# Performance work log

Measured on AMD Instinct MI355X. Metric: run time of the kernel, lower is better.

Reference implementation:

```python
import jax, jax.numpy as jnp
import numpy as np

N_NODES = 50000
N_EDGES = 800000
HIDDEN = 128
N_REL = 64
NUM_HEADS = 8
HEAD_DIM = HIDDEN // NUM_HEADS


def setup_inputs() -> dict:
    key = jax.random.key(0)
    ks = jax.random.split(key, 20)
    s = 0.05
    inp = {
        "x": jax.random.normal(ks[0], (N_NODES, HIDDEN), dtype=jnp.float32),
        "timestamps": jax.random.uniform(ks[1], (N_NODES,), dtype=jnp.float32),
        "src": jax.random.randint(ks[2], (N_EDGES,), 0, N_NODES),
        "dst": jax.random.randint(ks[3], (N_EDGES,), 0, N_NODES),
        "edge_type": jax.random.randint(ks[4], (N_EDGES,), 0, N_REL),
        "edge_time": jax.random.uniform(ks[5], (N_EDGES,), dtype=jnp.float32),
        # parameters (torch Linear stored as [in, out] so we use x @ W + b)
        "rel_table": jax.random.normal(ks[6], (N_REL, HIDDEN), dtype=jnp.float32) * s,
        "Wq": jax.random.normal(ks[7], (HIDDEN, HIDDEN), dtype=jnp.float32) * s,
        "bq": jnp.zeros((HIDDEN,), dtype=jnp.float32),
        "Wk": jax.random.normal(ks[8], (HIDDEN, HIDDEN), dtype=jnp.float32) * s,
        "bk": jnp.zeros((HIDDEN,), dtype=jnp.float32),
        "Wv": jax.random.normal(ks[9], (HIDDEN, HIDDEN), dtype=jnp.float32) * s,
        "bv": jnp.zeros((HIDDEN,), dtype=jnp.float32),
        "W1": jax.random.normal(ks[10], (2 * HIDDEN + 1, HIDDEN), dtype=jnp.float32) * s,
        "b1": jnp.zeros((HIDDEN,), dtype=jnp.float32),
        "W2": jax.random.normal(ks[11], (HIDDEN, 1), dtype=jnp.float32) * s,
        "b2": jnp.zeros((1,), dtype=jnp.float32),
        "time_coeff": jnp.array(1.0, dtype=jnp.float32),
    }
    return inp


def reference(x, timestamps, src, dst, edge_type, edge_time, rel_table,
              Wq, bq, Wk, bk, Wv, bv, W1, b1, W2, b2, time_coeff):
    N = x.shape[0]
    # temporal gating
    delta_t = (timestamps[dst] - edge_time) / (jnp.abs(time_coeff) + 1e-9)  # [E]
    time_mask = jax.nn.sigmoid(delta_t)[:, None]                            # [E,1]
    rel_emb = rel_table[edge_type] * time_mask                              # [E,H]
    src_emb = x[src]                                                        # [E,H]
    # dynamic edge weights: MLP([src_emb, rel_emb, time_mask]) -> sigmoid
    weight_input = jnp.concatenate([src_emb, rel_emb, time_mask], axis=-1)  # [E,2H+1]
    h = jax.nn.relu(weight_input @ W1 + b1)
    dynamic_weights = jax.nn.sigmoid(h @ W2 + b2)                           # [E,1]
    message = src_emb * rel_emb * dynamic_weights                           # [E,H]
    # multi-head edge attention keyed by dst
    q = (x[dst] @ Wq + bq).reshape(-1, NUM_HEADS, HEAD_DIM)
    k = (message @ Wk + bk).reshape(-1, NUM_HEADS, HEAD_DIM)
    v = (message @ Wv + bv).reshape(-1, NUM_HEADS, HEAD_DIM)
    scores = (q * k).sum(-1) / (HEAD_DIM ** 0.5)                            # [E,heads]
    # scatter softmax over edges grouped by dst
    seg_max = jax.ops.segment_max(scores, dst, num_segments=N)              # [N,heads]
    e = jnp.exp(scores - seg_max[dst])
    denom = jax.ops.segment_sum(e, dst, num_segments=N)
    attn = e / denom[dst]                                                   # [E,heads]
    out = jax.ops.segment_sum(v * attn[..., None], dst, num_segments=N)     # [N,heads,hd]
    return out.reshape(N, NUM_HEADS * HEAD_DIM)
```

## Files before the change

kernel.cpp:

```cpp
#include <hip/hip_runtime.h>

typedef __bf16 v8bf __attribute__((ext_vector_type(8)));
typedef __bf16 v4bf __attribute__((ext_vector_type(4)));
typedef float  v4f  __attribute__((ext_vector_type(4)));

#define MFMA16x16x32 __builtin_amdgcn_mfma_f32_16x16x32_bf16

#define HIDDEN 128
#define NHEADS 8

__global__ __launch_bounds__(256) void prep_hist(
    const float* __restrict__ rel, const float* __restrict__ W1,
    const float* __restrict__ Wk, const float* __restrict__ Wv,
    const float* __restrict__ W2, const int* __restrict__ dst,
    int* __restrict__ count,
    __bf16* __restrict__ mlppre, __bf16* __restrict__ relbf,
    __bf16* __restrict__ wswz, __bf16* __restrict__ w2bf, int E)
{
  const int b = blockIdx.x;
  if (b < 64) {
    __shared__ float rrow[128];
    const int j = threadIdx.x;
    if (j < 128) rrow[j] = rel[b*HIDDEN + j];
    __syncthreads();
    if (j < 128) {
      float acc = W1[256*HIDDEN + j];
      #pragma unroll 4
      for (int k=0;k<128;k++) acc += rrow[k]*W1[(128+k)*HIDDEN + j];
      mlppre[b*HIDDEN + j] = (__bf16)acc;
      relbf [b*HIDDEN + j] = (__bf16)rrow[j];
    }
  } else if (b < 80) {
    int f = (b - 64)*256 + threadIdx.x;
    if (f < 128) w2bf[f] = (__bf16)W2[f];
    if (f >= 2*8*4*64) return;
    int lane = f & 63, kk = (f>>6)&3, c = (f>>8)&7, mat = f>>11;
    const float* W = mat ? Wv : Wk;
    int qq = lane>>4, nn = lane&15;
    v8bf o;
    #pragma unroll
    for (int j=0;j<8;j++) o[j] = (__bf16)W[(kk*32 + qq*8 + j)*HIDDEN + c*16 + nn];
    *(v8bf*)(wswz + (long)f*8) = o;
  } else {
    long i = (long)(b - 80)*256 + threadIdx.x;
    long e4 = i*4;
    if (e4 + 3 < E) {
      int4 d = *(const int4*)(dst + e4);
      atomicAdd(&count[d.x], 1);
      atomicAdd(&count[d.y], 1);
      atomicAdd(&count[d.z], 1);
      atomicAdd(&count[d.w], 1);
    } else {
      for (long e = e4; e < E; e++) atomicAdd(&count[dst[e]], 1);
    }
  }
}

__global__ __launch_bounds__(1024) void scan_kernel(const int* __restrict__ count,
    int* __restrict__ base, int N)
{
  __shared__ int ssum[1024];
  const int t = threadIdx.x;
  const int chunk = (N + 1023) >> 10;
  const int lo = t*chunk, hi = min(lo + chunk, N);
  int s = 0;
  for (int i = lo; i < hi; i++) s += count[i];
  ssum[t] = s;
  __syncthreads();
  #pragma unroll
  for (int ofs = 1; ofs < 1024; ofs <<= 1) {
    int v = (t >= ofs) ? ssum[t - ofs] : 0;
    __syncthreads();
    ssum[t] += v;
    __syncthreads();
  }
  int run = (t == 0) ? 0 : ssum[t-1];
  for (int i = lo; i < hi; i++) { base[i] = run; run += count[i]; }
}

__global__ __launch_bounds__(512) void scat_pre(
    const float* __restrict__ x, const float* __restrict__ Wq,
    const float* __restrict__ bq, const float* __restrict__ W1,
    const float* __restrict__ b1,
    const int* __restrict__ src, const int* __restrict__ dstp,
    const int* __restrict__ etyp, const float* __restrict__ etime,
    const float* __restrict__ ts, const float* __restrict__ tc,
    const int* __restrict__ base, int* __restrict__ cursor,
    int4* __restrict__ meta4,
    __bf16* __restrict__ qbf, __bf16* __restrict__ hpre, __bf16* __restrict__ xbf,
    int N, int E, int SB)
{
  __shared__ __bf16 X[32][136];
  if ((int)blockIdx.x < SB) {
    int e = blockIdx.x*512 + threadIdx.x;
    if (e < E) {
      int d = dstp[e];
      int pI = base[d] + atomicAdd(&cursor[d], 1);
      float invtc = 1.0f / (fabsf(tc[0]) + 1e-9f);
      float dt = (ts[d] - etime[e]) * invtc;
      float tm = 1.0f/(1.0f + __expf(-dt));
      meta4[pI] = make_int4(src[e], d, etyp[e], __float_as_int(tm));
    }
    return;
  }
  const int pb = blockIdx.x - SB, npb = gridDim.x - SB;
  const int tid = threadIdx.x;
  const int w = tid >> 6, l = tid & 63, qd = l >> 4, ln = l & 15;
  const int col = w*16 + ln;

  v8bf BQ[4], BH[4];
  #pragma unroll
  for (int kk=0; kk<4; kk++) {
    v8bf f, g;
    #pragma unroll
    for (int j=0;j<8;j++){
      f[j] = (__bf16)Wq[(kk*32 + qd*8 + j)*HIDDEN + col];
      g[j] = (__bf16)W1[(kk*32 + qd*8 + j)*HIDDEN + col];
    }
    BQ[kk] = f; BH[kk] = g;
  }
  const float bqv = bq[col], b1v = b1[col];

  const int s = tid >> 4, c8 = (tid & 15)*8;
  for (int n0 = pb*32; n0 < N; n0 += npb*32) {
    __syncthreads();
    int n = n0 + s;
    v8bf xv;
    if (n < N) {
      const float4* xp = (const float4*)(x + (long)n*HIDDEN + c8);
      float4 a = xp[0], b = xp[1];
      xv[0]=(__bf16)a.x; xv[1]=(__bf16)a.y; xv[2]=(__bf16)a.z; xv[3]=(__bf16)a.w;
      xv[4]=(__bf16)b.x; xv[5]=(__bf16)b.y; xv[6]=(__bf16)b.z; xv[7]=(__bf16)b.w;
      *(v8bf*)(xbf + (long)n*HIDDEN + c8) = xv;
    } else {
      #pragma unroll
      for (int j=0;j<8;j++) xv[j] = (__bf16)0.f;
    }
    *(v8bf*)&X[s][c8] = xv;
    __syncthreads();

    v4f q0={0.f,0.f,0.f,0.f}, q1={0.f,0.f,0.f,0.f};
    v4f h0={0.f,0.f,0.f,0.f}, h1={0.f,0.f,0.f,0.f};
    #pragma unroll
    for (int kk=0;kk<4;kk++) {
      v8bf a0 = *(const v8bf*)&X[ln][kk*32 + qd*8];
      v8bf a1 = *(const v8bf*)&X[16+ln][kk*32 + qd*8];
      q0 = MFMA16x16x32(a0, BQ[kk], q0, 0,0,0);
      q1 = MFMA16x16x32(a1, BQ[kk], q1, 0,0,0);
      h0 = MFMA16x16x32(a0, BH[kk], h0, 0,0,0);
      h1 = MFMA16x16x32(a1, BH[kk], h1, 0,0,0);
    }
    #pragma unroll
    for (int r=0;r<4;r++) {
      int n_o = n0 + qd*4 + r;
      if (n_o < N) {
        qbf [(long)n_o*HIDDEN + col] = (__bf16)(q0[r] + bqv);
        hpre[(long)n_o*HIDDEN + col] = (__bf16)(h0[r] + b1v);
      }
      int n2 = n0 + 16 + qd*4 + r;
      if (n2 < N) {
        qbf [(long)n2*HIDDEN + col] = (__bf16)(q1[r] + bqv);
        hpre[(long)n2*HIDDEN + col] = (__bf16)(h1[r] + b1v);
      }
    }
  }
}

__global__ __launch_bounds__(256, 2) void edge_fused3(
    const int4* __restrict__ meta4, const float* __restrict__ b2,
    const __bf16* __restrict__ xbf, const __bf16* __restrict__ hpre,
    const __bf16* __restrict__ qbf, const __bf16* __restrict__ relbf,
    const __bf16* __restrict__ mlppre, const __bf16* __restrict__ w2bf,
    const __bf16* __restrict__ wswz,
    const float* __restrict__ bk, const float* __restrict__ bv,
    float* __restrict__ out, float* __restrict__ denom, int E, int ntiles)
{
  __shared__ __align__(16) __bf16 MSG[2][4096];

  const int tid = threadIdx.x;
  const int wid = tid >> 6, l = tid & 63, qd = l >> 4, ln = l & 15;
  const int le = l >> 3, lc = l & 7;

  v8bf bkf[2][4], bvf[2][4];
  #pragma unroll
  for (int c2=0;c2<2;c2++){
    const int c = wid*2 + c2;
    #pragma unroll
    for (int kk=0;kk<4;kk++){
      bkf[c2][kk] = *(const v8bf*)(wswz +         c*2048 + kk*512 + (size_t)l*8);
      bvf[c2][kk] = *(const v8bf*)(wswz + 16384 + c*2048 + kk*512 + (size_t)l*8);
    }
  }
  float bkC2[2], bvC2[2];
  #pragma unroll
  for (int c2=0;c2<2;c2++){
    bkC2[c2] = bk[(wid*2+c2)*16 + ln];
    bvC2[c2] = bv[(wid*2+c2)*16 + ln];
  }
  const float b2v = b2[0];
  const v8bf w2a = *(const v8bf*)(w2bf + lc*16);
  const v8bf w2b = *(const v8bf*)(w2bf + lc*16 + 8);

  const int g = gridDim.x;
  int t = blockIdx.x;
  if (t >= ntiles) return;

  int4 mt = make_int4(0, -1, 0, 0);
  { int e = t*32 + l; if (l < 32 && e < E) mt = meta4[e]; }
  int tn = t + g;
  int4 mtn = make_int4(0, -1, 0, 0);
  if (tn < ntiles) { int e = tn*32 + l; if (l < 32 && e < E) mtn = meta4[e]; }

  float tmE = __int_as_float(__shfl(mt.w, wid*8 + le));
  v8bf sv0, sv1, av0, av1, rv0, rv1, bp0, bp1;
  {
    int srcE = __shfl(mt.x, wid*8 + le);
    int tyE  = __shfl(mt.z, wid*8 + le);
    const __bf16* xs = xbf   + (long)srcE*HIDDEN + lc*16;
    const __bf16* hs = hpre  + (long)srcE*HIDDEN + lc*16;
    const __bf16* rs = relbf + (long)tyE *HIDDEN + lc*16;
    const __bf16* ms = mlppre+ (long)tyE *HIDDEN + lc*16;
    sv0 = *(const v8bf*)xs; sv1 = *(const v8bf*)(xs+8);
    av0 = *(const v8bf*)hs; av1 = *(const v8bf*)(hs+8);
    rv0 = *(const v8bf*)rs; rv1 = *(const v8bf*)(rs+8);
    bp0 = *(const v8bf*)ms; bp1 = *(const v8bf*)(ms+8);
  }
  float qA0[2][4], qA1[2][4];
  #pragma unroll
  for (int b=0;b<2;b++)
    #pragma unroll
    for (int r=0;r<4;r++){
      int d = __shfl(mt.y, b*16 + qd*4 + r);
      long drow = (long)(d < 0 ? 0 : d)*HIDDEN;
      qA0[b][r] = (float)qbf[drow + wid*32 + ln];
      qA1[b][r] = (float)qbf[drow + wid*32 + 16 + ln];
    }

  int p = 0;
  while (true) {
    const int d_m = mt.y;

    int dprev = __shfl(d_m, (l>0)?(l-1):0);
    int flag = (l < 32) && ((l==0) || (d_m != dprev));
    unsigned long long segmask = __ballot(flag);

    const int t2 = tn + g;
    int4 mt2 = make_int4(0, -1, 0, 0);
    if (t2 < ntiles) { int e = t2*32 + l; if (l < 32 && e < E) mt2 = meta4[e]; }

    const float tmN = __int_as_float(__shfl(mtn.w, wid*8 + le));
    const int srcN = __shfl(mtn.x, wid*8 + le);
    const int tyN  = __shfl(mtn.z, wid*8 + le);
    int dN[2][4];
    #pragma unroll
    for (int b=0;b<2;b++)
      #pragma unroll
      for (int r=0;r<4;r++) dN[b][r] = __shfl(mtn.y, b*16 + qd*4 + r);

    float z = 0.f;
    #pragma unroll
    for (int j=0;j<8;j++){
      float p0 = (float)av0[j] + tmE*(float)bp0[j];
      float p1 = (float)av1[j] + tmE*(float)bp1[j];
      z += fmaxf(p0,0.f)*(float)w2a[j] + fmaxf(p1,0.f)*(float)w2b[j];
    }
    z += __shfl_xor(z,1); z += __shfl_xor(z,2); z += __shfl_xor(z,4);
    const float dw = 1.0f/(1.0f + __expf(-(z + b2v)));
    const float sM = tmE * dw;

    {
      const int row = wid*8 + le;
      char* wbase = (char*)&MSG[p][0] + row*256;
      const int sw = (row & 7) << 4;
      v8bf m0, m1;
      #pragma unroll
      for (int j=0;j<8;j++){
        m0[j] = (__bf16)((float)sv0[j]*(float)rv0[j]*sM);
        m1[j] = (__bf16)((float)sv1[j]*(float)rv1[j]*sM);
      }
      *(v8bf*)(wbase + ((lc*32     ) ^ sw)) = m0;
      *(v8bf*)(wbase + ((lc*32 + 16) ^ sw)) = m1;
    }

    {
      const __bf16* xs = xbf   + (long)srcN*HIDDEN + lc*16;
      const __bf16* hs = hpre  + (long)srcN*HIDDEN + lc*16;
      const __bf16* rs = relbf + (long)tyN *HIDDEN + lc*16;
      const __bf16* ms = mlppre+ (long)tyN *HIDDEN + lc*16;
      sv0 = *(const v8bf*)xs; sv1 = *(const v8bf*)(xs+8);
      av0 = *(const v8bf*)hs; av1 = *(const v8bf*)(hs+8);
      rv0 = *(const v8bf*)rs; rv1 = *(const v8bf*)(rs+8);
      bp0 = *(const v8bf*)ms; bp1 = *(const v8bf*)(ms+8);
    }
    float qB0[2][4], qB1[2][4];
    #pragma unroll
    for (int b=0;b<2;b++)
      #pragma unroll
      for (int r=0;r<4;r++){
        int d = dN[b][r];
        long drow = (long)(d < 0 ? 0 : d)*HIDDEN;
        qB0[b][r] = (float)qbf[drow + wid*32 + ln];
        qB1[b][r] = (float)qbf[drow + wid*32 + 16 + ln];
      }

    asm volatile("s_waitcnt lgkmcnt(0)" ::: "memory");
    __builtin_amdgcn_s_barrier();

    const char* rb = (const char*)&MSG[p][0];
    v4f aK0[2], aK1[2], aV0[2], aV1[2];
    #pragma unroll
    for (int b=0;b<2;b++){
      const int rrow = b*16 + ln;
      const char* abase = rb + rrow*256;
      const int asw = (rrow & 7) << 4;
      v4f k0={0.f,0.f,0.f,0.f}, k1={0.f,0.f,0.f,0.f};
      v4f v0={0.f,0.f,0.f,0.f}, v1={0.f,0.f,0.f,0.f};
      #pragma unroll
      for (int kk=0;kk<4;kk++){
        v8bf a = *(const v8bf*)(abase + ((kk*64 + qd*16) ^ asw));
        k0 = MFMA16x16x32(a, bkf[0][kk], k0, 0,0,0);
        v0 = MFMA16x16x32(a, bvf[0][kk], v0, 0,0,0);
        k1 = MFMA16x16x32(a, bkf[1][kk], k1, 0,0,0);
        v1 = MFMA16x16x32(a, bvf[1][kk], v1, 0,0,0);
      }
      aK0[b]=k0; aK1[b]=k1; aV0[b]=v0; aV1[b]=v1;
    }

    float sc0[2][4], sc1[2][4];
    #pragma unroll
    for (int b=0;b<2;b++)
      #pragma unroll
      for (int r=0;r<4;r++){
        sc0[b][r] = (aK0[b][r] + bkC2[0])*qA0[b][r];
        sc1[b][r] = (aK1[b][r] + bkC2[1])*qA1[b][r];
      }
    #pragma unroll
    for (int m=1;m<16;m<<=1){
      #pragma unroll
      for (int b=0;b<2;b++)
        #pragma unroll
        for (int r=0;r<4;r++){
          sc0[b][r] += __shfl_xor(sc0[b][r], m);
          sc1[b][r] += __shfl_xor(sc1[b][r], m);
        }
    }
    float ee0[2][4], wv0[2][4], ee1[2][4], wv1[2][4];
    #pragma unroll
    for (int b=0;b<2;b++)
      #pragma unroll
      for (int r=0;r<4;r++){
        float e0_ = __expf(sc0[b][r]*0.25f);
        float e1_ = __expf(sc1[b][r]*0.25f);
        ee0[b][r] = e0_; wv0[b][r] = e0_*(aV0[b][r] + bvC2[0]);
        ee1[b][r] = e1_; wv1[b][r] = e1_*(aV1[b][r] + bvC2[1]);
      }

    unsigned long long mm = segmask;
    while (mm){
      int s0 = __ffsll((long long)mm) - 1;
      mm &= mm - 1;
      int s1 = mm ? (__ffsll((long long)mm) - 1) : 32;
      int dseg = __shfl(d_m, s0);
      if (dseg < 0) continue;
      float a0=0.f, a1=0.f, dn0=0.f, dn1=0.f;
      #pragma unroll
      for (int b=0;b<2;b++)
        #pragma unroll
        for (int r=0;r<4;r++){
          int rw = b*16 + qd*4 + r;
          bool in = (rw >= s0) && (rw < s1);
          a0  += in ? wv0[b][r] : 0.f;
          dn0 += in ? ee0[b][r] : 0.f;
          a1  += in ? wv1[b][r] : 0.f;
          dn1 += in ? ee1[b][r] : 0.f;
        }
      a0  += __shfl_xor(a0,16);  a0  += __shfl_xor(a0,32);
      a1  += __shfl_xor(a1,16);  a1  += __shfl_xor(a1,32);
      dn0 += __shfl_xor(dn0,16); dn0 += __shfl_xor(dn0,32);
      dn1 += __shfl_xor(dn1,16); dn1 += __shfl_xor(dn1,32);
      if (l < 16){
        atomicAdd(&out[(long)dseg*HIDDEN + wid*32 + ln], a0);
        atomicAdd(&out[(long)dseg*HIDDEN + wid*32 + 16 + ln], a1);
      }
      if (l == 0){
        atomicAdd(&denom[(long)dseg*NHEADS + wid*2    ], dn0);
        atomicAdd(&denom[(long)dseg*NHEADS + wid*2 + 1], dn1);
      }
    }

    if (tn >= ntiles) break;
    t = tn; tn = t2; mt = mtn; mtn = mt2; tmE = tmN;
    #pragma unroll
    for (int b=0;b<2;b++)
      #pragma unroll
      for (int r=0;r<4;r++){
        qA0[b][r] = qB0[b][r];
        qA1[b][r] = qB1[b][r];
      }
    p ^= 1;
  }
}

__global__ __launch_bounds__(512) void q_kernel(const float* __restrict__ x,
    const float* __restrict__ Wq, const float* __restrict__ bq,
    float* __restrict__ q, int N)
{
  __shared__ __bf16 X[32][136];
  const int tid = threadIdx.x;
  const int w = tid >> 6, l = tid & 63, qd = l >> 4, ln = l & 15;
  const int col = w*16 + ln;
  v8bf B[4];
  #pragma unroll
  for (int kk=0; kk<4; kk++) {
    v8bf f;
    #pragma unroll
    for (int j=0;j<8;j++) f[j] = (__bf16)Wq[(kk*32 + qd*8 + j)*HIDDEN + col];
    B[kk] = f;
  }
  const float bqv = bq[col];
  const int s = tid >> 4, c8 = (tid & 15)*8;
  for (int n0 = blockIdx.x*32; n0 < N; n0 += gridDim.x*32) {
    __syncthreads();
    int n = n0 + s;
    v8bf xv;
    if (n < N) {
      const float4* xp = (const float4*)(x + (long)n*HIDDEN + c8);
      float4 a = xp[0], b = xp[1];
      xv[0]=(__bf16)a.x; xv[1]=(__bf16)a.y; xv[2]=(__bf16)a.z; xv[3]=(__bf16)a.w;
      xv[4]=(__bf16)b.x; xv[5]=(__bf16)b.y; xv[6]=(__bf16)b.z; xv[7]=(__bf16)b.w;
    } else {
      #pragma unroll
      for (int j=0;j<8;j++) xv[j] = (__bf16)0.f;
    }
    *(v8bf*)&X[s][c8] = xv;
    __syncthreads();
    v4f acc0 = {0.f,0.f,0.f,0.f}, acc1 = {0.f,0.f,0.f,0.f};
    #pragma unroll
    for (int kk=0;kk<4;kk++) {
      v8bf a0 = *(const v8bf*)&X[ln][kk*32 + qd*8];
      v8bf a1 = *(const v8bf*)&X[16+ln][kk*32 + qd*8];
      acc0 = MFMA16x16x32(a0, B[kk], acc0, 0,0,0);
      acc1 = MFMA16x16x32(a1, B[kk], acc1, 0,0,0);
    }
    #pragma unroll
    for (int r=0;r<4;r++) {
      int n_o = n0 + qd*4 + r;
      if (n_o < N) q[(long)n_o*HIDDEN + col] = acc0[r] + bqv;
      int n_o2 = n0 + 16 + qd*4 + r;
      if (n_o2 < N) q[(long)n_o2*HIDDEN + col] = acc1[r] + bqv;
    }
  }
}

__global__ __launch_bounds__(512) void edge_atomic(
    const float* __restrict__ x, const float* __restrict__ ts,
    const int* __restrict__ src, const int* __restrict__ dst,
    const int* __restrict__ etyp, const float* __restrict__ etime,
    const float* __restrict__ rel,
    const float* __restrict__ Wk, const float* __restrict__ bk,
    const float* __restrict__ Wv, const float* __restrict__ bv,
    const float* __restrict__ W1, const float* __restrict__ b1,
    const float* __restrict__ W2, const float* __restrict__ b2,
    const float* __restrict__ tc,
    const float* __restrict__ qws, float* __restrict__ denom,
    float* __restrict__ out, int E)
{
  __shared__ __bf16 A[32][264];
  __shared__ __bf16 A2[32][136];
  __shared__ float sW2[128], sb1[128], sw1r[128], sbk[128], sbv[128];
  __shared__ float stm[32], sdw[32];
  __shared__ int   ssrc[32], sdst[32], styp[32];
  __shared__ float dwpart[8][32];
  const int tid = threadIdx.x;
  const int w = tid >> 6, l = tid & 63, qd = l >> 4, ln = l & 15;
  const int col = w*16 + ln;
  v8bf B1[8], BK[4], BV[4];
  #pragma unroll
  for (int kk=0;kk<8;kk++){ v8bf f;
    #pragma unroll
    for (int j=0;j<8;j++) f[j] = (__bf16)W1[(kk*32+qd*8+j)*HIDDEN + col];
    B1[kk]=f; }
  #pragma unroll
  for (int kk=0;kk<4;kk++){ v8bf f,g;
    #pragma unroll
    for (int j=0;j<8;j++){ f[j] = (__bf16)Wk[(kk*32+qd*8+j)*HIDDEN + col];
                           g[j] = (__bf16)Wv[(kk*32+qd*8+j)*HIDDEN + col]; }
    BK[kk]=f; BV[kk]=g; }
  if (tid < 128) {
    sW2[tid]=W2[tid]; sb1[tid]=b1[tid]; sw1r[tid]=W1[256*HIDDEN+tid];
    sbk[tid]=bk[tid]; sbv[tid]=bv[tid];
  }
  const float b2v = b2[0];
  const float invtc = 1.0f / (fabsf(tc[0]) + 1e-9f);
  const int s = tid >> 4, c8 = (tid & 15)*8;
  const int ntiles = (E + 31) >> 5;
  for (int t = blockIdx.x; t < ntiles; t += gridDim.x) {
    const int e0 = t*32;
    __syncthreads();
    if (tid < 32) {
      int e = e0 + tid;
      if (e < E) {
        int d = dst[e];
        ssrc[tid]=src[e]; sdst[tid]=d; styp[tid]=etyp[e];
        float dt = (ts[d] - etime[e]) * invtc;
        stm[tid] = 1.0f/(1.0f+expf(-dt));
      } else { ssrc[tid]=0; sdst[tid]=0; styp[tid]=0; stm[tid]=0.f; }
    }
    __syncthreads();
    {
      const float tmv = stm[s];
      const float4* xp = (const float4*)(x + (long)ssrc[s]*HIDDEN + c8);
      float4 a = xp[0], b = xp[1];
      const float4* rp = (const float4*)(rel + (long)styp[s]*HIDDEN + c8);
      float4 ra = rp[0], rb = rp[1];
      v8bf sv, rv;
      sv[0]=(__bf16)a.x; sv[1]=(__bf16)a.y; sv[2]=(__bf16)a.z; sv[3]=(__bf16)a.w;
      sv[4]=(__bf16)b.x; sv[5]=(__bf16)b.y; sv[6]=(__bf16)b.z; sv[7]=(__bf16)b.w;
      rv[0]=(__bf16)(ra.x*tmv); rv[1]=(__bf16)(ra.y*tmv);
      rv[2]=(__bf16)(ra.z*tmv); rv[3]=(__bf16)(ra.w*tmv);
      rv[4]=(__bf16)(rb.x*tmv); rv[5]=(__bf16)(rb.y*tmv);
      rv[6]=(__bf16)(rb.z*tmv); rv[7]=(__bf16)(rb.w*tmv);
      *(v8bf*)&A[s][c8] = sv;
      *(v8bf*)&A[s][128 + c8] = rv;
    }
    __syncthreads();
    v4f acc0={0.f,0.f,0.f,0.f}, acc1={0.f,0.f,0.f,0.f};
    #pragma unroll
    for (int kk=0;kk<8;kk++){
      v8bf a0 = *(const v8bf*)&A[ln][kk*32 + qd*8];
      v8bf a1 = *(const v8bf*)&A[16+ln][kk*32 + qd*8];
      acc0 = MFMA16x16x32(a0, B1[kk], acc0, 0,0,0);
      acc1 = MFMA16x16x32(a1, B1[kk], acc1, 0,0,0);
    }
    float part[8];
    {
      const float w1rj = sw1r[col], b1j = sb1[col], w2j = sW2[col];
      #pragma unroll
      for (int r=0;r<4;r++){
        int i0 = qd*4 + r, i1 = 16 + qd*4 + r;
        part[r]   = fmaxf(acc0[r] + stm[i0]*w1rj + b1j, 0.f)*w2j;
        part[4+r] = fmaxf(acc1[r] + stm[i1]*w1rj + b1j, 0.f)*w2j;
      }
    }
    #pragma unroll
    for (int m=1;m<16;m<<=1){
      #pragma unroll
      for (int i=0;i<8;i++) part[i] += __shfl_xor(part[i], m, 16);
    }
    if (ln == 0){
      #pragma unroll
      for (int r=0;r<4;r++){ dwpart[w][qd*4+r]=part[r]; dwpart[w][16+qd*4+r]=part[4+r]; }
    }
    __syncthreads();
    if (tid < 32){
      float z = b2v;
      #pragma unroll
      for (int ww=0;ww<8;ww++) z += dwpart[ww][tid];
      sdw[tid] = 1.0f/(1.0f+expf(-z));
    }
    __syncthreads();
    {
      const float dwv = sdw[s];
      v8bf mv;
      #pragma unroll
      for (int i=0;i<8;i++)
        mv[i] = (__bf16)((float)A[s][c8+i]*(float)A[s][128+c8+i]*dwv);
      *(v8bf*)&A2[s][c8] = mv;
    }
    __syncthreads();
    v4f k0={0.f,0.f,0.f,0.f}, k1={0.f,0.f,0.f,0.f};
    v4f v0={0.f,0.f,0.f,0.f}, v1={0.f,0.f,0.f,0.f};
    #pragma unroll
    for (int kk=0;kk<4;kk++){
      v8bf a0 = *(const v8bf*)&A2[ln][kk*32 + qd*8];
      v8bf a1 = *(const v8bf*)&A2[16+ln][kk*32 + qd*8];
      k0 = MFMA16x16x32(a0, BK[kk], k0, 0,0,0);
      k1 = MFMA16x16x32(a1, BK[kk], k1, 0,0,0);
      v0 = MFMA16x16x32(a0, BV[kk], v0, 0,0,0);
      v1 = MFMA16x16x32(a1, BV[kk], v1, 0,0,0);
    }
    float sc[8];
    const float bkj = sbk[col], bvj = sbv[col];
    #pragma unroll
    for (int r=0;r<4;r++){
      int i0 = qd*4 + r, i1 = 16 + qd*4 + r;
      sc[r]   = (k0[r]+bkj)*qws[(long)sdst[i0]*HIDDEN + col];
      sc[4+r] = (k1[r]+bkj)*qws[(long)sdst[i1]*HIDDEN + col];
    }
    #pragma unroll
    for (int m=1;m<16;m<<=1){
      #pragma unroll
      for (int i=0;i<8;i++) sc[i] += __shfl_xor(sc[i], m, 16);
    }
    float ee[8];
    #pragma unroll
    for (int i=0;i<8;i++) ee[i] = expf(sc[i]*0.25f);
    if (ln == 0){
      #pragma unroll
      for (int r=0;r<4;r++){
        int i0 = qd*4 + r, i1 = 16 + qd*4 + r;
        if (e0+i0 < E) atomicAdd(&denom[(long)sdst[i0]*NHEADS + w], ee[r]);
        if (e0+i1 < E) atomicAdd(&denom[(long)sdst[i1]*NHEADS + w], ee[4+r]);
      }
    }
    #pragma unroll
    for (int r=0;r<4;r++){
      int i0 = qd*4 + r, i1 = 16 + qd*4 + r;
      if (e0+i0 < E) atomicAdd(&out[(long)sdst[i0]*HIDDEN + col], ee[r]*(v0[r]+bvj));
      if (e0+i1 < E) atomicAdd(&out[(long)sdst[i1]*HIDDEN + col], ee[4+r]*(v1[r]+bvj));
    }
  }
}

__global__ void fin_kernel(float* __restrict__ out, const float* __restrict__ denom, int N)
{
  int idx = blockIdx.x*blockDim.x + threadIdx.x;
  int total = N*32;
  if (idx < total){
    int n = idx >> 5;
    int h = (idx & 31) >> 2;
    float d = denom[n*8 + h];
    float inv = d > 0.f ? 1.0f/d : 0.f;
    float4* p = (float4*)out + idx;
    float4 v = *p;
    v.x*=inv; v.y*=inv; v.z*=inv; v.w*=inv;
    *p = v;
  }
}

static inline size_t align256(size_t v){ return (v + 255) & ~(size_t)255; }

extern "C" void kernel_launch(void* const* d_in, const int* in_sizes, int n_in,
                              void* d_out, int out_size, void* d_ws, size_t ws_size,
                              hipStream_t stream)
{
  const float* x      = (const float*)d_in[0];
  const float* ts     = (const float*)d_in[1];
  const int*   src    = (const int*)d_in[2];
  const int*   dstp   = (const int*)d_in[3];
  const int*   etyp   = (const int*)d_in[4];
  const float* etime  = (const float*)d_in[5];
  const float* rel    = (const float*)d_in[6];
  const float* Wq     = (const float*)d_in[7];
  const float* bq     = (const float*)d_in[8];
  const float* Wk     = (const float*)d_in[9];
  const float* bk     = (const float*)d_in[10];
  const float* Wv     = (const float*)d_in[11];
  const float* bv     = (const float*)d_in[12];
  const float* W1     = (const float*)d_in[13];
  const float* b1     = (const float*)d_in[14];
  const float* W2     = (const float*)d_in[15];
  const float* b2     = (const float*)d_in[16];
  const float* tc     = (const float*)d_in[17];
  float* out = (float*)d_out;

  const int N = in_sizes[0] / HIDDEN;
  const int E = in_sizes[2];

  char* ws = (char*)d_ws;
  size_t off = 0;
  __bf16* qbf    = (__bf16*)(ws + off); off += align256((size_t)N*HIDDEN*2);
  __bf16* hpre   = (__bf16*)(ws + off); off += align256((size_t)N*HIDDEN*2);
  __bf16* xbf    = (__bf16*)(ws + off); off += align256((size_t)N*HIDDEN*2);
  __bf16* relbf  = (__bf16*)(ws + off); off += align256((size_t)64*HIDDEN*2);
  __bf16* mlppre = (__bf16*)(ws + off); off += align256((size_t)64*HIDDEN*2);
  __bf16* w2bf   = (__bf16*)(ws + off); off += align256((size_t)HIDDEN*2);
  __bf16* wswz   = (__bf16*)(ws + off); off += align256((size_t)4096*8*2);
  size_t zoff = off;
  int*    countp = (int*)(ws + off);    off += align256((size_t)N*4);
  int*    cursor = (int*)(ws + off);    off += align256((size_t)N*4);
  float*  denom  = (float*)(ws + off);  off += align256((size_t)N*NHEADS*4);
  size_t zlen = off - zoff;
  int4*   meta4  = (int4*)(ws + off);   off += align256((size_t)E*16);
  int*    basep  = (int*)(ws + off);    off += align256((size_t)N*4);
  const size_t needed_fast = off;

  if (ws_size >= needed_fast) {
    hipMemsetAsync(ws + zoff, 0, zlen, stream);
    hipMemsetAsync(out, 0, (size_t)N*HIDDEN*4, stream);

    const int haBlocks = 80 + (E + 1023)/1024;
    prep_hist<<<haBlocks, 256, 0, stream>>>(rel, W1, Wk, Wv, W2, dstp, countp,
        mlppre, relbf, wswz, w2bf, E);
    scan_kernel<<<1, 1024, 0, stream>>>(countp, basep, N);
    const int SB = (E + 511)/512;
    scat_pre<<<SB + 1024, 512, 0, stream>>>(x, Wq, bq, W1, b1,
        src, dstp, etyp, etime, ts, tc, basep, cursor, meta4,
        qbf, hpre, xbf, N, E, SB);

    const int ntiles = (E + 31) >> 5;
    edge_fused3<<<2048, 256, 0, stream>>>(meta4, b2,
        xbf, hpre, qbf, relbf, mlppre, w2bf, wswz, bk, bv, out, denom, E, ntiles);
    fin_kernel<<<(N*32 + 255)/256, 256, 0, stream>>>(out, denom, N);
  } else {
    float* qws    = (float*)ws;
    float* denom2 = (float*)(ws + align256((size_t)N*HIDDEN*4));
    hipMemsetAsync(out,    0, (size_t)N*HIDDEN*4, stream);
    hipMemsetAsync(denom2, 0, (size_t)N*NHEADS*4, stream);
    q_kernel<<<512, 512, 0, stream>>>(x, Wq, bq, qws, N);
    edge_atomic<<<512, 512, 0, stream>>>(x, ts, src, dstp, etyp, etime, rel,
        Wk, bk, Wv, bv, W1, b1, W2, b2, tc, qws, denom2, out, E);
    fin_kernel<<<(N*32 + 255)/256, 256, 0, stream>>>(out, denom2, N);
  }
}
```

Measured before the change: 526.3 us.

## Restructure edge kernel to one head per wave with 512-thread blocks

```diff
diff --git a/kernel.cpp b/kernel.cpp
--- a/kernel.cpp
+++ b/kernel.cpp
@@ -15,7 +15,8 @@
     const float* __restrict__ W2, const int* __restrict__ dst,
     int* __restrict__ count,
     __bf16* __restrict__ mlppre, __bf16* __restrict__ relbf,
-    __bf16* __restrict__ wswz, __bf16* __restrict__ w2bf, int E)
+    __bf16* __restrict__ wswz, __bf16* __restrict__ w2bf,
+    float* __restrict__ outz, int E, int hb, int nz4)
 {
   const int b = blockIdx.x;
   if (b < 64) {
@@ -41,7 +42,7 @@
     #pragma unroll
     for (int j=0;j<8;j++) o[j] = (__bf16)W[(kk*32 + qq*8 + j)*HIDDEN + c*16 + nn];
     *(v8bf*)(wswz + (long)f*8) = o;
-  } else {
+  } else if (b < 80 + hb) {
     long i = (long)(b - 80)*256 + threadIdx.x;
     long e4 = i*4;
     if (e4 + 3 < E) {
@@ -53,6 +54,9 @@
     } else {
       for (long e = e4; e < E; e++) atomicAdd(&count[dst[e]], 1);
     }
+  } else {
+    int idx = (b - 80 - hb)*256 + threadIdx.x;
+    if (idx < nz4) ((float4*)outz)[idx] = make_float4(0.f,0.f,0.f,0.f);
   }
 }
 
@@ -61,10 +65,15 @@
 {
   __shared__ int ssum[1024];
   const int t = threadIdx.x;
-  const int chunk = (N + 1023) >> 10;
+  const int chunk = ((N + 4095) >> 12) << 2;
   const int lo = t*chunk, hi = min(lo + chunk, N);
   int s = 0;
-  for (int i = lo; i < hi; i++) s += count[i];
+  int i = lo;
+  for (; i + 3 < hi; i += 4) {
+    int4 v = *(const int4*)(count + i);
+    s += v.x + v.y + v.z + v.w;
+  }
+  for (; i < hi; i++) s += count[i];
   ssum[t] = s;
   __syncthreads();
   #pragma unroll
@@ -75,7 +84,15 @@
     __syncthreads();
   }
   int run = (t == 0) ? 0 : ssum[t-1];
-  for (int i = lo; i < hi; i++) { base[i] = run; run += count[i]; }
+  i = lo;
+  for (; i + 3 < hi; i += 4) {
+    int4 c = *(const int4*)(count + i);
+    int4 o;
+    o.x = run; o.y = run + c.x; o.z = o.y + c.y; o.w = o.z + c.z;
+    *(int4*)(base + i) = o;
+    run = o.w + c.w;
+  }
+  for (; i < hi; i++) { base[i] = run; run += count[i]; }
 }
 
 __global__ __launch_bounds__(512) void scat_pre(
@@ -166,7 +183,7 @@
   }
 }
 
-__global__ __launch_bounds__(256, 2) void edge_fused3(
+__global__ __launch_bounds__(512, 4) void edge_fused4(
     const int4* __restrict__ meta4, const float* __restrict__ b2,
     const __bf16* __restrict__ xbf, const __bf16* __restrict__ hpre,
     const __bf16* __restrict__ qbf, const __bf16* __restrict__ relbf,
@@ -179,27 +196,19 @@
 
   const int tid = threadIdx.x;
   const int wid = tid >> 6, l = tid & 63, qd = l >> 4, ln = l & 15;
-  const int le = l >> 3, lc = l & 7;
-
-  v8bf bkf[2][4], bvf[2][4];
+  const int eIdx = wid*4 + (l >> 4);
+  const int lc = l & 15;
+
+  v8bf bkf[4], bvf[4];
   #pragma unroll
-  for (int c2=0;c2<2;c2++){
-    const int c = wid*2 + c2;
-    #pragma unroll
-    for (int kk=0;kk<4;kk++){
-      bkf[c2][kk] = *(const v8bf*)(wswz +         c*2048 + kk*512 + (size_t)l*8);
-      bvf[c2][kk] = *(const v8bf*)(wswz + 16384 + c*2048 + kk*512 + (size_t)l*8);
-    }
-  }
-  float bkC2[2], bvC2[2];
-  #pragma unroll
-  for (int c2=0;c2<2;c2++){
-    bkC2[c2] = bk[(wid*2+c2)*16 + ln];
-    bvC2[c2] = bv[(wid*2+c2)*16 + ln];
-  }
+  for (int kk=0;kk<4;kk++){
+    bkf[kk] = *(const v8bf*)(wswz +         wid*2048 + kk*512 + (size_t)l*8);
+    bvf[kk] = *(const v8bf*)(wswz + 16384 + wid*2048 + kk*512 + (size_t)l*8);
+  }
+  const float bkc = bk[wid*16 + ln];
+  const float bvc = bv[wid*16 + ln];
   const float b2v = b2[0];
-  const v8bf w2a = *(const v8bf*)(w2bf + lc*16);
-  const v8bf w2b = *(const v8bf*)(w2bf + lc*16 + 8);
+  const v8bf w2v = *(const v8bf*)(w2bf + lc*8);
 
   const int g = gridDim.x;
   int t = blockIdx.x;
@@ -211,30 +220,16 @@
   int4 mtn = make_int4(0, -1, 0, 0);
   if (tn < ntiles) { int e = tn*32 + l; if (l < 32 && e < E) mtn = meta4[e]; }
 
-  float tmE = __int_as_float(__shfl(mt.w, wid*8 + le));
-  v8bf sv0, sv1, av0, av1, rv0, rv1, bp0, bp1;
+  float tmE = __int_as_float(__shfl(mt.w, eIdx));
+  v8bf sv, av, rv, bp;
   {
-    int srcE = __shfl(mt.x, wid*8 + le);
-    int tyE  = __shfl(mt.z, wid*8 + le);
-    const __bf16* xs = xbf   + (long)srcE*HIDDEN + lc*16;
-    const __bf16* hs = hpre  + (long)srcE*HIDDEN + lc*16;
-    const __bf16* rs = relbf + (long)tyE *HIDDEN + lc*16;
-    const __bf16* ms = mlppre+ (long)tyE *HIDDEN + lc*16;
-    sv0 = *(const v8bf*)xs; sv1 = *(const v8bf*)(xs+8);
-    av0 = *(const v8bf*)hs; av1 = *(const v8bf*)(hs+8);
-    rv0 = *(const v8bf*)rs; rv1 = *(const v8bf*)(rs+8);
-    bp0 = *(const v8bf*)ms; bp1 = *(const v8bf*)(ms+8);
-  }
-  float qA0[2][4], qA1[2][4];
-  #pragma unroll
-  for (int b=0;b<2;b++)
-    #pragma unroll
-    for (int r=0;r<4;r++){
-      int d = __shfl(mt.y, b*16 + qd*4 + r);
-      long drow = (long)(d < 0 ? 0 : d)*HIDDEN;
-      qA0[b][r] = (float)qbf[drow + wid*32 + ln];
-      qA1[b][r] = (float)qbf[drow + wid*32 + 16 + ln];
-    }
+    int srcE = __shfl(mt.x, eIdx);
+    int tyE  = __shfl(mt.z, eIdx);
+    sv = *(const v8bf*)(xbf   + (long)srcE*HIDDEN + lc*8);
+    av = *(const v8bf*)(hpre  + (long)srcE*HIDDEN + lc*8);
+    rv = *(const v8bf*)(relbf + (long)tyE *HIDDEN + lc*8);
+    bp = *(const v8bf*)(mlppre+ (long)tyE *HIDDEN + lc*8);
+  }
 
   int p = 0;
   while (true) {
@@ -244,115 +239,96 @@
     int flag = (l < 32) && ((l==0) || (d_m != dprev));
     unsigned long long segmask = __ballot(flag);
 
+    int dC[2][4];
+    #pragma unroll
+    for (int b=0;b<2;b++)
+      #pragma unroll
+      for (int r=0;r<4;r++) dC[b][r] = __shfl(d_m, b*16 + qd*4 + r);
+
     const int t2 = tn + g;
     int4 mt2 = make_int4(0, -1, 0, 0);
     if (t2 < ntiles) { int e = t2*32 + l; if (l < 32 && e < E) mt2 = meta4[e]; }
 
-    const float tmN = __int_as_float(__shfl(mtn.w, wid*8 + le));
-    const int srcN = __shfl(mtn.x, wid*8 + le);
-    const int tyN  = __shfl(mtn.z, wid*8 + le);
-    int dN[2][4];
-    #pragma unroll
-    for (int b=0;b<2;b++)
-      #pragma unroll
-      for (int r=0;r<4;r++) dN[b][r] = __shfl(mtn.y, b*16 + qd*4 + r);
+    const float tmN = __int_as_float(__shfl(mtn.w, eIdx));
+    const int srcN = __shfl(mtn.x, eIdx);
+    const int tyN  = __shfl(mtn.z, eIdx);
 
     float z = 0.f;
     #pragma unroll
     for (int j=0;j<8;j++){
-      float p0 = (float)av0[j] + tmE*(float)bp0[j];
-      float p1 = (float)av1[j] + tmE*(float)bp1[j];
-      z += fmaxf(p0,0.f)*(float)w2a[j] + fmaxf(p1,0.f)*(float)w2b[j];
-    }
-    z += __shfl_xor(z,1); z += __shfl_xor(z,2); z += __shfl_xor(z,4);
+      float pj = (float)av[j] + tmE*(float)bp[j];
+      z += fmaxf(pj, 0.f)*(float)w2v[j];
+    }
+    z += __shfl_xor(z,1); z += __shfl_xor(z,2);
+    z += __shfl_xor(z,4); z += __shfl_xor(z,8);
     const float dw = 1.0f/(1.0f + __expf(-(z + b2v)));
     const float sM = tmE * dw;
 
     {
-      const int row = wid*8 + le;
-      char* wbase = (char*)&MSG[p][0] + row*256;
-      const int sw = (row & 7) << 4;
-      v8bf m0, m1;
-      #pragma unroll
-      for (int j=0;j<8;j++){
-        m0[j] = (__bf16)((float)sv0[j]*(float)rv0[j]*sM);
-        m1[j] = (__bf16)((float)sv1[j]*(float)rv1[j]*sM);
-      }
-      *(v8bf*)(wbase + ((lc*32     ) ^ sw)) = m0;
-      *(v8bf*)(wbase + ((lc*32 + 16) ^ sw)) = m1;
-    }
-
-    {
-      const __bf16* xs = xbf   + (long)srcN*HIDDEN + lc*16;
-      const __bf16* hs = hpre  + (long)srcN*HIDDEN + lc*16;
-      const __bf16* rs = relbf + (long)tyN *HIDDEN + lc*16;
-      const __bf16* ms = mlppre+ (long)tyN *HIDDEN + lc*16;
-      sv0 = *(const v8bf*)xs; sv1 = *(const v8bf*)(xs+8);
-      av0 = *(const v8bf*)hs; av1 = *(const v8bf*)(hs+8);
-      rv0 = *(const v8bf*)rs; rv1 = *(const v8bf*)(rs+8);
-      bp0 = *(const v8bf*)ms; bp1 = *(const v8bf*)(ms+8);
-    }
-    float qB0[2][4], qB1[2][4];
-    #pragma unroll
-    for (int b=0;b<2;b++)
-      #pragma unroll
-      for (int r=0;r<4;r++){
-        int d = dN[b][r];
-        long drow = (long)(d < 0 ? 0 : d)*HIDDEN;
-        qB0[b][r] = (float)qbf[drow + wid*32 + ln];
-        qB1[b][r] = (float)qbf[drow + wid*32 + 16 + ln];
-      }
+      char* wbase = (char*)&MSG[p][0] + eIdx*256;
+      const int sw = (eIdx & 7) << 4;
+      v8bf m;
+      #pragma unroll
+      for (int j=0;j<8;j++) m[j] = (__bf16)((float)sv[j]*(float)rv[j]*sM);
+      *(v8bf*)(wbase + ((lc*16) ^ sw)) = m;
+    }
+
+    sv = *(const v8bf*)(xbf   + (long)srcN*HIDDEN + lc*8);
+    av = *(const v8bf*)(hpre  + (long)srcN*HIDDEN + lc*8);
+    rv = *(const v8bf*)(relbf + (long)tyN *HIDDEN + lc*8);
+    bp = *(const v8bf*)(mlppre+ (long)tyN *HIDDEN + lc*8);
 
     asm volatile("s_waitcnt lgkmcnt(0)" ::: "memory");
     __builtin_amdgcn_s_barrier();
 
+    float qv[2][4];
+    #pragma unroll
+    for (int b=0;b<2;b++)
+      #pragma unroll
+      for (int r=0;r<4;r++){
+        int d = dC[b][r];
+        qv[b][r] = (float)qbf[(long)(d<0?0:d)*HIDDEN + wid*16 + ln];
+      }
+
     const char* rb = (const char*)&MSG[p][0];
-    v4f aK0[2], aK1[2], aV0[2], aV1[2];
+    v4f aK[2], aV[2];
+    __builtin_amdgcn_s_setprio(1);
     #pragma unroll
     for (int b=0;b<2;b++){
       const int rrow = b*16 + ln;
       const char* abase = rb + rrow*256;
       const int asw = (rrow & 7) << 4;
-      v4f k0={0.f,0.f,0.f,0.f}, k1={0.f,0.f,0.f,0.f};
-      v4f v0={0.f,0.f,0.f,0.f}, v1={0.f,0.f,0.f,0.f};
+      v4f k_ = {0.f,0.f,0.f,0.f}, v_ = {0.f,0.f,0.f,0.f};
       #pragma unroll
       for (int kk=0;kk<4;kk++){
         v8bf a = *(const v8bf*)(abase + ((kk*64 + qd*16) ^ asw));
-        k0 = MFMA16x16x32(a, bkf[0][kk], k0, 0,0,0);
-        v0 = MFMA16x16x32(a, bvf[0][kk], v0, 0,0,0);
-        k1 = MFMA16x16x32(a, bkf[1][kk], k1, 0,0,0);
-        v1 = MFMA16x16x32(a, bvf[1][kk], v1, 0,0,0);
+        k_ = MFMA16x16x32(a, bkf[kk], k_, 0,0,0);
+        v_ = MFMA16x16x32(a, bvf[kk], v_, 0,0,0);
       }
-      aK0[b]=k0; aK1[b]=k1; aV0[b]=v0; aV1[b]=v1;
-    }
-
-    float sc0[2][4], sc1[2][4];
+      aK[b] = k_; aV[b] = v_;
+    }
+    __builtin_amdgcn_s_setprio(0);
+
+    float sc[2][4];
     #pragma unroll
     for (int b=0;b<2;b++)
       #pragma unroll
-      for (int r=0;r<4;r++){
-        sc0[b][r] = (aK0[b][r] + bkC2[0])*qA0[b][r];
-        sc1[b][r] = (aK1[b][r] + bkC2[1])*qA1[b][r];
-      }
+      for (int r=0;r<4;r++) sc[b][r] = (aK[b][r] + bkc)*qv[b][r];
     #pragma unroll
     for (int m=1;m<16;m<<=1){
       #pragma unroll
       for (int b=0;b<2;b++)
         #pragma unroll
-        for (int r=0;r<4;r++){
-          sc0[b][r] += __shfl_xor(sc0[b][r], m);
-          sc1[b][r] += __shfl_xor(sc1[b][r], m);
-        }
-    }
-    float ee0[2][4], wv0[2][4], ee1[2][4], wv1[2][4];
+        for (int r=0;r<4;r++) sc[b][r] += __shfl_xor(sc[b][r], m);
+    }
+    float ee[2][4], wv[2][4];
     #pragma unroll
     for (int b=0;b<2;b++)
       #pragma unroll
       for (int r=0;r<4;r++){
-        float e0_ = __expf(sc0[b][r]*0.25f);
-        float e1_ = __expf(sc1[b][r]*0.25f);
-        ee0[b][r] = e0_; wv0[b][r] = e0_*(aV0[b][r] + bvC2[0]);
-        ee1[b][r] = e1_; wv1[b][r] = e1_*(aV1[b][r] + bvC2[1]);
+        float e_ = __expf(sc[b][r]*0.25f);
+        ee[b][r] = e_;
+        wv[b][r] = e_*(aV[b][r] + bvc);
       }
 
     unsigned long long mm = segmask;
@@ -362,41 +338,24 @@
       int s1 = mm ? (__ffsll((long long)mm) - 1) : 32;
       int dseg = __shfl(d_m, s0);
       if (dseg < 0) continue;
-      float a0=0.f, a1=0.f, dn0=0.f, dn1=0.f;
+      float a0 = 0.f, dn0 = 0.f;
       #pragma unroll
       for (int b=0;b<2;b++)
         #pragma unroll
         for (int r=0;r<4;r++){
           int rw = b*16 + qd*4 + r;
           bool in = (rw >= s0) && (rw < s1);
-          a0  += in ? wv0[b][r] : 0.f;
-          dn0 += in ? ee0[b][r] : 0.f;
-          a1  += in ? wv1[b][r] : 0.f;
-          dn1 += in ? ee1[b][r] : 0.f;
+          a0  += in ? wv[b][r] : 0.f;
+          dn0 += in ? ee[b][r] : 0.f;
         }
       a0  += __shfl_xor(a0,16);  a0  += __shfl_xor(a0,32);
-      a1  += __shfl_xor(a1,16);  a1  += __shfl_xor(a1,32);
       dn0 += __shfl_xor(dn0,16); dn0 += __shfl_xor(dn0,32);
-      dn1 += __shfl_xor(dn1,16); dn1 += __shfl_xor(dn1,32);
-      if (l < 16){
-        atomicAdd(&out[(long)dseg*HIDDEN + wid*32 + ln], a0);
-        atomicAdd(&out[(long)dseg*HIDDEN + wid*32 + 16 + ln], a1);
-      }
-      if (l == 0){
-        atomicAdd(&denom[(long)dseg*NHEADS + wid*2    ], dn0);
-        atomicAdd(&denom[(long)dseg*NHEADS + wid*2 + 1], dn1);
-      }
+      if (l < 16) atomicAdd(&out[(long)dseg*HIDDEN + wid*16 + ln], a0);
+      if (l == 0) atomicAdd(&denom[(long)dseg*NHEADS + wid], dn0);
     }
 
     if (tn >= ntiles) break;
     t = tn; tn = t2; mt = mtn; mtn = mt2; tmE = tmN;
-    #pragma unroll
-    for (int b=0;b<2;b++)
-      #pragma unroll
-      for (int r=0;r<4;r++){
-        qA0[b][r] = qB0[b][r];
-        qA1[b][r] = qB1[b][r];
-      }
     p ^= 1;
   }
 }
@@ -677,11 +636,12 @@
 
   if (ws_size >= needed_fast) {
     hipMemsetAsync(ws + zoff, 0, zlen, stream);
-    hipMemsetAsync(out, 0, (size_t)N*HIDDEN*4, stream);
-
-    const int haBlocks = 80 + (E + 1023)/1024;
-    prep_hist<<<haBlocks, 256, 0, stream>>>(rel, W1, Wk, Wv, W2, dstp, countp,
-        mlppre, relbf, wswz, w2bf, E);
+
+    const int hb = (E + 1023)/1024;
+    const int nz4 = N*32;
+    const int zb = (nz4 + 255)/256;
+    prep_hist<<<80 + hb + zb, 256, 0, stream>>>(rel, W1, Wk, Wv, W2, dstp, countp,
+        mlppre, relbf, wswz, w2bf, out, E, hb, nz4);
     scan_kernel<<<1, 1024, 0, stream>>>(countp, basep, N);
     const int SB = (E + 511)/512;
     scat_pre<<<SB + 1024, 512, 0, stream>>>(x, Wq, bq, W1, b1,
@@ -689,7 +649,7 @@
         qbf, hpre, xbf, N, E, SB);
 
     const int ntiles = (E + 31) >> 5;
-    edge_fused3<<<2048, 256, 0, stream>>>(meta4, b2,
+    edge_fused4<<<1024, 512, 0, stream>>>(meta4, b2,
         xbf, hpre, qbf, relbf, mlppre, w2bf, wswz, bk, bv, out, denom, E, ntiles);
     fin_kernel<<<(N*32 + 255)/256, 256, 0, stream>>>(out, denom, N);
   } else {
```

After: 505.8 us. -3.9%, faster.
